# Kernel optimization log

Measured on AMD Instinct MI355X. Metric: run time of the kernel, lower is better.

## Reference

```python
import jax, jax.numpy as jnp
import numpy as np

B, P, CIN = 512, 64, 512       # batch, h*w feature positions, resnet18 channels
HID, EMB, NCLS, T = 512, 512, 96, 30


def setup_inputs() -> dict:
    key = jax.random.key(0)
    ks = jax.random.split(key, 16)
    s = 0.02
    return {
        "features": jax.random.normal(ks[0], (B, P, CIN), jnp.float32),
        "targets": jax.random.randint(ks[1], (B, T), 0, NCLS),
        "max_length": T,
        "Wfc": jax.random.normal(ks[2], (HID, CIN), jnp.float32) * s,
        "bfc": jnp.zeros((HID,), jnp.float32),
        "emb_table": jax.random.normal(ks[3], (NCLS, EMB), jnp.float32) * s,
        "Wa": jax.random.normal(ks[4], (HID, HID + EMB), jnp.float32) * s,
        "ba": jnp.zeros((HID,), jnp.float32),
        "Wc": jax.random.normal(ks[5], (HID, HID + EMB), jnp.float32) * s,
        "bc": jnp.zeros((HID,), jnp.float32),
        "Wih": jax.random.normal(ks[6], (4 * HID, HID), jnp.float32) * s,
        "Whh": jax.random.normal(ks[7], (4 * HID, HID), jnp.float32) * s,
        "bih": jnp.zeros((4 * HID,), jnp.float32),
        "bhh": jnp.zeros((4 * HID,), jnp.float32),
        "Wo": jax.random.normal(ks[8], (NCLS, HID), jnp.float32) * s,
        "bo": jnp.zeros((NCLS,), jnp.float32),
    }


def reference(features, targets, max_length, Wfc, bfc, emb_table, Wa, ba,
              Wc, bc, Wih, Whh, bih, bhh, Wo, bo):
    b = features.shape[0]
    hid = Wfc.shape[0]
    feats = features @ Wfc.T + bfc                       # [b, P, hid]
    # teacher forcing: input at t=0 is token 0, then targets[:, t-1]
    in_ids = jnp.concatenate(
        [jnp.zeros((b, 1), targets.dtype), targets[:, : max_length - 1]], axis=1)
    emb_seq = emb_table[in_ids].transpose(1, 0, 2)       # [T, b, emb]

    def step(carry, emb):
        h, c = carry
        # first softmax is over the hidden dim (as in the original module)
        a = jax.nn.softmax(jnp.concatenate([h, emb], -1) @ Wa.T + ba, axis=-1)  # [b,hid]
        scores = jnp.einsum('bph,bh->bp', feats, a)      # [b, P]
        w = jax.nn.softmax(scores, axis=-1)
        ctx = jnp.einsum('bp,bph->bh', w, feats)         # [b, hid]
        x = jnp.concatenate([emb, ctx], -1) @ Wc.T + bc  # [b, hid]
        gates = x @ Wih.T + bih + h @ Whh.T + bhh        # [b, 4*hid]
        i, f, g, o = jnp.split(gates, 4, axis=-1)        # torch gate order i,f,g,o
        c_new = jax.nn.sigmoid(f) * c + jax.nn.sigmoid(i) * jnp.tanh(g)
        h_new = jax.nn.sigmoid(o) * jnp.tanh(c_new)
        out = h_new @ Wo.T + bo                          # [b, ncls]
        return (h_new, c_new), out

    h0 = jnp.zeros((b, hid), feats.dtype)
    (_, _), outs = jax.lax.scan(step, (h0, h0), emb_seq)
    return outs.transpose(1, 0, 2)                       # [b, T, ncls]
```

## Files before the change

kernel.cpp:

```cpp
#include <hip/hip_runtime.h>
#include <math.h>

static constexpr int BATCH = 512;
static constexpr int PPOS  = 64;
static constexpr int HIDC  = 512;

typedef __attribute__((ext_vector_type(8))) short bf8;
typedef __attribute__((ext_vector_type(4))) float f4;

static __device__ __forceinline__ float sigmoidf_(float x) { return 1.f / (1.f + expf(-x)); }

static __device__ __forceinline__ short f2bf(float x) {
  unsigned u = __float_as_uint(x);
  u = u + 0x7FFF + ((u >> 16) & 1);
  return (short)(u >> 16);
}
static __device__ __forceinline__ float bf2f(short s) {
  return __uint_as_float(((unsigned)(unsigned short)s) << 16);
}

__global__ void transpose_k(const float* __restrict__ src, float* __restrict__ dst, int R, int C, int ld) {
  __shared__ float tile[32][33];
  int c0 = blockIdx.x * 32, r0 = blockIdx.y * 32;
  int x = threadIdx.x;
  for (int yy = threadIdx.y; yy < 32; yy += 8) {
    int r = r0 + yy, c = c0 + x;
    if (r < R && c < C) tile[yy][x] = src[(size_t)r * ld + c];
  }
  __syncthreads();
  for (int yy = threadIdx.y; yy < 32; yy += 8) {
    int c = c0 + yy, r = r0 + x;
    if (r < R && c < C) dst[(size_t)c * R + r] = tile[x][yy];
  }
}

__global__ void bfuse_k(const float* __restrict__ Wih, const float* __restrict__ bc,
                        const float* __restrict__ bih, const float* __restrict__ bhh,
                        float* __restrict__ bf) {
  int n = blockIdx.x * 256 + threadIdx.x;
  float s = bih[n] + bhh[n];
  const float* w = Wih + (size_t)n * 512;
  for (int m = 0; m < 512; m++) s += w[m] * bc[m];
  bf[n] = s;
}

__global__ void split_k(const float* __restrict__ src, short* __restrict__ hi, short* __restrict__ lo, int n) {
  int i = blockIdx.x * 256 + threadIdx.x;
  if (i < n) {
    float x = src[i];
    short h = f2bf(x);
    hi[i] = h;
    lo[i] = f2bf(x - bf2f(h));
  }
}

__global__ void pack_split_k(const float* __restrict__ src, int ld,
                             short* __restrict__ hi, short* __restrict__ lo) {
  int idx = blockIdx.x * 256 + threadIdx.x;
  int j = idx & 7, lane = (idx >> 3) & 63, kf = (idx >> 9) & 15, cg = idx >> 13;
  int n = cg * 16 + (lane & 15);
  int k = kf * 32 + ((lane >> 4) << 3) + j;
  float v = src[(size_t)n * ld + k];
  short h = f2bf(v);
  hi[idx] = h;
  lo[idx] = f2bf(v - bf2f(h));
}

__global__ void build_btg_pack_k(const float* __restrict__ tmp, const float* __restrict__ Whh,
                                 short* __restrict__ hi, short* __restrict__ lo) {
  int idx = blockIdx.x * 256 + threadIdx.x;
  int j = idx & 7, lane = (idx >> 3) & 63, kf = (idx >> 9) & 31, cg = idx >> 14;
  int cp = cg * 16 + (lane & 15);
  int k = kf * 32 + ((lane >> 4) << 3) + j;
  int jj = cp >> 2, g = cp & 3;
  int n = g * 512 + jj;
  float v = (k < 512) ? tmp[(size_t)(512 + k) * 2048 + n] : Whh[(size_t)n * 512 + (k - 512)];
  short h = f2bf(v);
  hi[idx] = h;
  lo[idx] = f2bf(v - bf2f(h));
}

__global__ __launch_bounds__(256) void gemb_k(const float* __restrict__ emb_table, const float* __restrict__ tmp,
                                              const float* __restrict__ bfused, float* __restrict__ Gemb_p) {
  __shared__ float emb_s[4][512];
  int tid = threadIdx.x;
  int n0 = blockIdx.x * 256;
  int e0 = blockIdx.y * 4;
  for (int i = tid; i < 2048; i += 256)
    emb_s[i >> 9][i & 511] = emb_table[(size_t)(e0 + (i >> 9)) * 512 + (i & 511)];
  __syncthreads();
  int n = n0 + tid;
  float acc[4] = {};
  for (int k = 0; k < 512; k++) {
    float w = tmp[(size_t)k * 2048 + n];
#pragma unroll
    for (int e = 0; e < 4; e++) acc[e] += emb_s[e][k] * w;
  }
  int cp = (n & 511) * 4 + (n >> 9);
  float b = bfused[n];
#pragma unroll
  for (int e = 0; e < 4; e++) Gemb_p[(size_t)(e0 + e) * 2048 + cp] = acc[e] + b;
}

__global__ __launch_bounds__(256) void za_k(const float* __restrict__ emb_table, const float* __restrict__ WaT_emb,
                                            const float* __restrict__ ba, float* __restrict__ Za) {
  __shared__ float emb_s[4][512];
  int tid = threadIdx.x;
  int n0 = blockIdx.x * 256;
  int e0 = blockIdx.y * 4;
  for (int i = tid; i < 2048; i += 256)
    emb_s[i >> 9][i & 511] = emb_table[(size_t)(e0 + (i >> 9)) * 512 + (i & 511)];
  __syncthreads();
  int n = n0 + tid;
  float acc[4] = {};
  for (int k = 0; k < 512; k++) {
    float w = WaT_emb[(size_t)k * 512 + n];
#pragma unroll
    for (int e = 0; e < 4; e++) acc[e] += emb_s[e][k] * w;
  }
  float b = ba[n];
#pragma unroll
  for (int e = 0; e < 4; e++) Za[(size_t)(e0 + e) * 512 + n] = acc[e] + b;
}

__global__ __launch_bounds__(256) void feats_mfma_k(const float* __restrict__ A,
                                                    const short* __restrict__ Ph, const short* __restrict__ Pl,
                                                    const float* __restrict__ bias, float* __restrict__ C) {
  __shared__ short Ah[2][64][40], Al[2][64][40];
  int blk = blockIdx.x;
  int xt = (blk >> 3) & 3;
  int ytile = (blk >> 5) * 8 + (blk & 7);
  int row0 = ytile * 64, col0 = xt * 128;
  int tid = threadIdx.x;
  int lane = tid & 63, wave = tid >> 6;
  int wm = (wave & 1) * 32, wn = (wave >> 1) * 64;
  int r15 = lane & 15, q8 = (lane >> 4) * 8;
  int smA = tid >> 2, skA = (tid & 3) * 8;
  const float* Ap = A + (size_t)(row0 + smA) * 512 + skA;
  int cg0 = (col0 + wn) >> 4;
  const short* pbh = Ph + (size_t)cg0 * 8192 + lane * 8;
  const short* pbl = Pl + (size_t)cg0 * 8192 + lane * 8;
  float4 a0 = *(const float4*)Ap, a1 = *(const float4*)(Ap + 4);
  bf8 bhc[4], blc[4], bhn[4], bln[4];
#pragma unroll
  for (int c = 0; c < 4; c++) {
    bhc[c] = *(const bf8*)(pbh + c * 8192);
    blc[c] = *(const bf8*)(pbl + c * 8192);
  }
  f4 acc[2][4] = {};
#pragma unroll 2
  for (int kt = 0; kt < 16; kt++) {
    int buf = kt & 1;
    {
      float av[8] = {a0.x, a0.y, a0.z, a0.w, a1.x, a1.y, a1.z, a1.w};
      bf8 ahv, alv;
#pragma unroll
      for (int i = 0; i < 8; i++) {
        short h = f2bf(av[i]);
        ahv[i] = h;
        alv[i] = f2bf(av[i] - bf2f(h));
      }
      *(bf8*)&Ah[buf][smA][skA] = ahv;
      *(bf8*)&Al[buf][smA][skA] = alv;
    }
    if (kt + 1 < 16) {
      Ap += 32;
      a0 = *(const float4*)Ap; a1 = *(const float4*)(Ap + 4);
#pragma unroll
      for (int c = 0; c < 4; c++) {
        bhn[c] = *(const bf8*)(pbh + c * 8192 + (kt + 1) * 512);
        bln[c] = *(const bf8*)(pbl + c * 8192 + (kt + 1) * 512);
      }
    }
    __syncthreads();
    bf8 fah[2], fal[2];
#pragma unroll
    for (int r = 0; r < 2; r++) {
      fah[r] = *(const bf8*)&Ah[buf][wm + r * 16 + r15][q8];
      fal[r] = *(const bf8*)&Al[buf][wm + r * 16 + r15][q8];
    }
#pragma unroll
    for (int r = 0; r < 2; r++)
#pragma unroll
      for (int c = 0; c < 4; c++) {
        acc[r][c] = __builtin_amdgcn_mfma_f32_16x16x32_bf16(fah[r], bhc[c], acc[r][c], 0, 0, 0);
        acc[r][c] = __builtin_amdgcn_mfma_f32_16x16x32_bf16(fal[r], bhc[c], acc[r][c], 0, 0, 0);
        acc[r][c] = __builtin_amdgcn_mfma_f32_16x16x32_bf16(fah[r], blc[c], acc[r][c], 0, 0, 0);
      }
#pragma unroll
    for (int c = 0; c < 4; c++) { bhc[c] = bhn[c]; blc[c] = bln[c]; }
  }
#pragma unroll
  for (int r = 0; r < 2; r++)
#pragma unroll
    for (int c = 0; c < 4; c++) {
      int col = col0 + wn + c * 16 + r15;
      float bv = bias[col];
#pragma unroll
      for (int i = 0; i < 4; i++) {
        int row = row0 + wm + r * 16 + (lane >> 4) * 4 + i;
        C[(size_t)row * 512 + col] = acc[r][c][i] + bv;
      }
    }
}

__global__ __launch_bounds__(256) void tmp_mfma_k(const float* __restrict__ A,
                                                  const short* __restrict__ BTh, const short* __restrict__ BTl,
                                                  float* __restrict__ C) {
  __shared__ short Ah[2][64][40], Al[2][64][40], Bh[2][128][40], Bl[2][128][40];
  int row0 = blockIdx.y * 64, col0 = blockIdx.x * 128;
  int tid = threadIdx.x;
  int lane = tid & 63, wave = tid >> 6;
  int wm = (wave & 1) * 32, wn = (wave >> 1) * 64;
  int r15 = lane & 15, q8 = (lane >> 4) * 8;
  int smA = tid >> 2, skA = (tid & 3) * 8;
  int smB = tid >> 1, skB = (tid & 1) * 16;
  const float* Ap = A + (size_t)(row0 + smA) * 512 + skA;
  const short* Bhp = BTh + (size_t)(col0 + smB) * 512 + skB;
  const short* Blp = BTl + (size_t)(col0 + smB) * 512 + skB;
  float4 a0 = *(const float4*)Ap, a1 = *(const float4*)(Ap + 4);
  bf8 bh0 = *(const bf8*)Bhp, bh1 = *(const bf8*)(Bhp + 8);
  bf8 bl0 = *(const bf8*)Blp, bl1 = *(const bf8*)(Blp + 8);
  f4 acc[2][4] = {};
  for (int kt = 0; kt < 16; kt++) {
    int buf = kt & 1;
    {
      float av[8] = {a0.x, a0.y, a0.z, a0.w, a1.x, a1.y, a1.z, a1.w};
      bf8 ahv, alv;
#pragma unroll
      for (int i = 0; i < 8; i++) {
        short h = f2bf(av[i]);
        ahv[i] = h;
        alv[i] = f2bf(av[i] - bf2f(h));
      }
      *(bf8*)&Ah[buf][smA][skA] = ahv;
      *(bf8*)&Al[buf][smA][skA] = alv;
      *(bf8*)&Bh[buf][smB][skB] = bh0;
      *(bf8*)&Bh[buf][smB][skB + 8] = bh1;
      *(bf8*)&Bl[buf][smB][skB] = bl0;
      *(bf8*)&Bl[buf][smB][skB + 8] = bl1;
    }
    if (kt + 1 < 16) {
      Ap += 32; Bhp += 32; Blp += 32;
      a0 = *(const float4*)Ap; a1 = *(const float4*)(Ap + 4);
      bh0 = *(const bf8*)Bhp; bh1 = *(const bf8*)(Bhp + 8);
      bl0 = *(const bf8*)Blp; bl1 = *(const bf8*)(Blp + 8);
    }
    __syncthreads();
    bf8 fah[2], fal[2], fbh[4], fbl[4];
#pragma unroll
    for (int r = 0; r < 2; r++) {
      fah[r] = *(const bf8*)&Ah[buf][wm + r * 16 + r15][q8];
      fal[r] = *(const bf8*)&Al[buf][wm + r * 16 + r15][q8];
    }
#pragma unroll
    for (int c = 0; c < 4; c++) {
      fbh[c] = *(const bf8*)&Bh[buf][wn + c * 16 + r15][q8];
      fbl[c] = *(const bf8*)&Bl[buf][wn + c * 16 + r15][q8];
    }
#pragma unroll
    for (int r = 0; r < 2; r++)
#pragma unroll
      for (int c = 0; c < 4; c++) {
        acc[r][c] = __builtin_amdgcn_mfma_f32_16x16x32_bf16(fah[r], fbh[c], acc[r][c], 0, 0, 0);
        acc[r][c] = __builtin_amdgcn_mfma_f32_16x16x32_bf16(fal[r], fbh[c], acc[r][c], 0, 0, 0);
        acc[r][c] = __builtin_amdgcn_mfma_f32_16x16x32_bf16(fah[r], fbl[c], acc[r][c], 0, 0, 0);
      }
  }
#pragma unroll
  for (int r = 0; r < 2; r++)
#pragma unroll
    for (int c = 0; c < 4; c++) {
      int col = col0 + wn + c * 16 + r15;
#pragma unroll
      for (int i = 0; i < 4; i++) {
        int row = row0 + wm + r * 16 + (lane >> 4) * 4 + i;
        C[(size_t)row * 2048 + col] = acc[r][c][i];
      }
    }
}

__global__ __launch_bounds__(256) void z_mfma_k(const short* __restrict__ h_hi, const short* __restrict__ h_lo,
                                                const short* __restrict__ Ph, const short* __restrict__ Pl,
                                                float* __restrict__ zbuf) {
  __shared__ short Ah[2][32][72], Al[2][32][72];
  int tid = threadIdx.x;
  int lane = tid & 63, wave = tid >> 6;
  int wm = (wave & 1) * 16, wn = (wave >> 1) * 16;
  int r15 = lane & 15, q4 = (lane >> 4) * 4, q8 = (lane >> 4) * 8;
  int row0 = blockIdx.y * 32, col0 = blockIdx.x * 32;
  int kz = blockIdx.z * 256;
  int sm = tid >> 3, sk = (tid & 7) * 8;
  const short* ahp = h_hi + (size_t)(row0 + sm) * 512 + kz + sk;
  const short* alp = h_lo + (size_t)(row0 + sm) * 512 + kz + sk;
  int cg = (col0 + wn) >> 4;
  const short* pbh = Ph + (size_t)cg * 8192 + (size_t)blockIdx.z * 8 * 512 + lane * 8;
  const short* pbl = Pl + (size_t)cg * 8192 + (size_t)blockIdx.z * 8 * 512 + lane * 8;
  bf8 ah = *(const bf8*)ahp, al = *(const bf8*)alp;
  bf8 bhc[2], blc[2], bhn[2], bln[2];
#pragma unroll
  for (int ks = 0; ks < 2; ks++) {
    bhc[ks] = *(const bf8*)(pbh + ks * 512);
    blc[ks] = *(const bf8*)(pbl + ks * 512);
  }
  f4 acc = {};
#pragma unroll 2
  for (int kt = 0; kt < 4; kt++) {
    int buf = kt & 1;
    *(bf8*)&Ah[buf][sm][sk] = ah;
    *(bf8*)&Al[buf][sm][sk] = al;
    if (kt + 1 < 4) {
      ahp += 64; alp += 64;
      ah = *(const bf8*)ahp; al = *(const bf8*)alp;
#pragma unroll
      for (int ks = 0; ks < 2; ks++) {
        bhn[ks] = *(const bf8*)(pbh + ((kt + 1) * 2 + ks) * 512);
        bln[ks] = *(const bf8*)(pbl + ((kt + 1) * 2 + ks) * 512);
      }
    }
    __syncthreads();
#pragma unroll
    for (int ks = 0; ks < 2; ks++) {
      bf8 fah = *(const bf8*)&Ah[buf][wm + r15][ks * 32 + q8];
      bf8 fal = *(const bf8*)&Al[buf][wm + r15][ks * 32 + q8];
      acc = __builtin_amdgcn_mfma_f32_16x16x32_bf16(fah, bhc[ks], acc, 0, 0, 0);
      acc = __builtin_amdgcn_mfma_f32_16x16x32_bf16(fal, bhc[ks], acc, 0, 0, 0);
      acc = __builtin_amdgcn_mfma_f32_16x16x32_bf16(fah, blc[ks], acc, 0, 0, 0);
    }
#pragma unroll
    for (int ks = 0; ks < 2; ks++) { bhc[ks] = bhn[ks]; blc[ks] = bln[ks]; }
  }
  float* zo = zbuf + (size_t)blockIdx.z * (512 * 512);
  int col = col0 + wn + r15;
#pragma unroll
  for (int i = 0; i < 4; i++)
    zo[(size_t)(row0 + wm + q4 + i) * 512 + col] = acc[i];
}

__global__ __launch_bounds__(512) void attn_fin_k(const float* __restrict__ zbuf,
                                                  const int* __restrict__ targets, int t, int T,
                                                  const float* __restrict__ Za, const float* __restrict__ feats,
                                                  short* __restrict__ ctx_hi, short* __restrict__ ctx_lo) {
  __shared__ float a_s[512];
  __shared__ float redm[8], reds[8];
  __shared__ float sc_s[64];
  __shared__ float w_s[64];
  __shared__ float cpart[8][512];
  int tid = threadIdx.x;
  int wid = tid >> 6, lane = tid & 63;
  int b = blockIdx.x;
  int id = (t == 0) ? 0 : targets[b * T + t - 1];

  const float4* fbase = (const float4*)(feats + (size_t)b * PPOS * 512);
  float4 f1[8], f2[8];
#pragma unroll
  for (int q = 0; q < 8; q++) {
    int p = wid * 8 + q;
    f1[q] = fbase[(size_t)p * 128 + lane];
    f2[q] = fbase[(size_t)p * 128 + 64 + lane];
  }

  float zv = zbuf[(size_t)b * 512 + tid] + zbuf[(size_t)(512 * 512) + b * 512 + tid]
           + Za[(size_t)id * 512 + tid];
  float m = zv;
#pragma unroll
  for (int off = 32; off; off >>= 1) m = fmaxf(m, __shfl_xor(m, off, 64));
  if (lane == 0) redm[wid] = m;
  __syncthreads();
  float M = redm[0];
#pragma unroll
  for (int w = 1; w < 8; w++) M = fmaxf(M, redm[w]);
  float e = expf(zv - M);
  float s = e;
#pragma unroll
  for (int off = 32; off; off >>= 1) s += __shfl_xor(s, off, 64);
  if (lane == 0) reds[wid] = s;
  __syncthreads();
  float S = 0.f;
#pragma unroll
  for (int w = 0; w < 8; w++) S += reds[w];
  a_s[tid] = e * (1.f / S);
  __syncthreads();

  float4 a1 = ((const float4*)a_s)[lane];
  float4 a2 = ((const float4*)a_s)[lane + 64];
#pragma unroll
  for (int q = 0; q < 8; q++) {
    float d = f1[q].x * a1.x + f1[q].y * a1.y + f1[q].z * a1.z + f1[q].w * a1.w
            + f2[q].x * a2.x + f2[q].y * a2.y + f2[q].z * a2.z + f2[q].w * a2.w;
#pragma unroll
    for (int off = 32; off; off >>= 1) d += __shfl_xor(d, off, 64);
    if (lane == 0) sc_s[wid * 8 + q] = d;
  }
  __syncthreads();

  if (wid == 0) {
    float v = sc_s[lane];
    float mm = v;
#pragma unroll
    for (int off = 32; off; off >>= 1) mm = fmaxf(mm, __shfl_xor(mm, off, 64));
    float ee = expf(v - mm);
    float ss = ee;
#pragma unroll
    for (int off = 32; off; off >>= 1) ss += __shfl_xor(ss, off, 64);
    w_s[lane] = ee / ss;
  }
  __syncthreads();

  float4 c1 = {0.f, 0.f, 0.f, 0.f}, c2 = {0.f, 0.f, 0.f, 0.f};
#pragma unroll
  for (int q = 0; q < 8; q++) {
    float wp = w_s[wid * 8 + q];
    c1.x += wp * f1[q].x; c1.y += wp * f1[q].y; c1.z += wp * f1[q].z; c1.w += wp * f1[q].w;
    c2.x += wp * f2[q].x; c2.y += wp * f2[q].y; c2.z += wp * f2[q].z; c2.w += wp * f2[q].w;
  }
  ((float4*)&cpart[wid][0])[lane] = c1;
  ((float4*)&cpart[wid][256])[lane] = c2;
  __syncthreads();

  float acc = 0.f;
#pragma unroll
  for (int w = 0; w < 8; w++) acc += cpart[w][tid];
  short hh = f2bf(acc);
  ctx_hi[(size_t)b * 512 + tid] = hh;
  ctx_lo[(size_t)b * 512 + tid] = f2bf(acc - bf2f(hh));
}

__global__ __launch_bounds__(256) void gates_mfma_k(const short* __restrict__ ctx_hi, const short* __restrict__ ctx_lo,
                                                    const short* __restrict__ h_hi_in, const short* __restrict__ h_lo_in,
                                                    const int* __restrict__ targets, int t, int T,
                                                    const short* __restrict__ Ph, const short* __restrict__ Pl,
                                                    const float* __restrict__ Gemb_p,
                                                    float* __restrict__ cbuf, float* __restrict__ h_new,
                                                    short* __restrict__ h_hi_out, short* __restrict__ h_lo_out) {
  __shared__ short Ah[2][32][72], Al[2][32][72];
  __shared__ float Cs[32][68];
  int tid = threadIdx.x;
  int lane = tid & 63, wave = tid >> 6;
  int wn = wave * 16;
  int r15 = lane & 15, q8 = (lane >> 4) * 8;
  int row0 = blockIdx.y * 32, col0 = blockIdx.x * 64;
  int smA = tid >> 3, skA = (tid & 7) * 8;
  const short* actx_h = ctx_hi + (size_t)(row0 + smA) * 512;
  const short* actx_l = ctx_lo + (size_t)(row0 + smA) * 512;
  const short* ahst_h = h_hi_in + (size_t)(row0 + smA) * 512;
  const short* ahst_l = h_lo_in + (size_t)(row0 + smA) * 512;
  int cg = (col0 >> 4) + wave;
  const short* pbh = Ph + (size_t)cg * 16384 + lane * 8;
  const short* pbl = Pl + (size_t)cg * 16384 + lane * 8;
  bf8 ah = *(const bf8*)(actx_h + skA), al = *(const bf8*)(actx_l + skA);
  bf8 bhc[2], blc[2], bhn[2], bln[2];
#pragma unroll
  for (int ks = 0; ks < 2; ks++) {
    bhc[ks] = *(const bf8*)(pbh + ks * 512);
    blc[ks] = *(const bf8*)(pbl + ks * 512);
  }
  f4 acc[2] = {};
#pragma unroll 2
  for (int kt = 0; kt < 16; kt++) {
    int buf = kt & 1;
    *(bf8*)&Ah[buf][smA][skA] = ah;
    *(bf8*)&Al[buf][smA][skA] = al;
    if (kt + 1 < 16) {
      int kk = (kt + 1) * 64 + skA;
      if (kk < 512) {
        ah = *(const bf8*)(actx_h + kk);
        al = *(const bf8*)(actx_l + kk);
      } else {
        ah = *(const bf8*)(ahst_h + kk - 512);
        al = *(const bf8*)(ahst_l + kk - 512);
      }
#pragma unroll
      for (int ks = 0; ks < 2; ks++) {
        bhn[ks] = *(const bf8*)(pbh + ((kt + 1) * 2 + ks) * 512);
        bln[ks] = *(const bf8*)(pbl + ((kt + 1) * 2 + ks) * 512);
      }
    }
    __syncthreads();
#pragma unroll
    for (int ks = 0; ks < 2; ks++) {
      bf8 fah[2], fal[2];
#pragma unroll
      for (int r = 0; r < 2; r++) {
        fah[r] = *(const bf8*)&Ah[buf][r * 16 + r15][ks * 32 + q8];
        fal[r] = *(const bf8*)&Al[buf][r * 16 + r15][ks * 32 + q8];
      }
#pragma unroll
      for (int r = 0; r < 2; r++) {
        acc[r] = __builtin_amdgcn_mfma_f32_16x16x32_bf16(fah[r], bhc[ks], acc[r], 0, 0, 0);
        acc[r] = __builtin_amdgcn_mfma_f32_16x16x32_bf16(fal[r], bhc[ks], acc[r], 0, 0, 0);
        acc[r] = __builtin_amdgcn_mfma_f32_16x16x32_bf16(fah[r], blc[ks], acc[r], 0, 0, 0);
      }
    }
#pragma unroll
    for (int ks = 0; ks < 2; ks++) { bhc[ks] = bhn[ks]; blc[ks] = bln[ks]; }
  }
#pragma unroll
  for (int r = 0; r < 2; r++)
#pragma unroll
    for (int i = 0; i < 4; i++)
      Cs[r * 16 + (lane >> 4) * 4 + i][wn + r15] = acc[r][i];
  __syncthreads();
#pragma unroll
  for (int it = 0; it < 2; it++) {
    int idx = it * 256 + tid;
    int row = idx >> 4, jj = idx & 15;
    int b = row0 + row;
    int jg = (col0 >> 2) + jj;
    int id = (t == 0) ? 0 : targets[b * T + t - 1];
    float4 g4 = *(const float4*)(Gemb_p + (size_t)id * 2048 + col0 + jj * 4);
    float ig = sigmoidf_(Cs[row][jj * 4 + 0] + g4.x);
    float fg = sigmoidf_(Cs[row][jj * 4 + 1] + g4.y);
    float gg = tanhf(Cs[row][jj * 4 + 2] + g4.z);
    float og = sigmoidf_(Cs[row][jj * 4 + 3] + g4.w);
    float cn = fg * cbuf[(size_t)b * 512 + jg] + ig * gg;
    float hn = og * tanhf(cn);
    cbuf[(size_t)b * 512 + jg] = cn;
    h_new[(size_t)b * 512 + jg] = hn;
    short hh = f2bf(hn);
    h_hi_out[(size_t)b * 512 + jg] = hh;
    h_lo_out[(size_t)b * 512 + jg] = f2bf(hn - bf2f(hh));
  }
}

__global__ __launch_bounds__(256) void out_gemm_k(const float* __restrict__ h_hist, const float* __restrict__ WoT,
                                                  const float* __restrict__ bo, float* __restrict__ out, int T) {
  __shared__ float As[16][68];
  __shared__ float Bs[16][96];
  int tid = threadIdx.x;
  int tx = tid & 15, ty = tid >> 4;
  int row0 = blockIdx.x * 64;
  float acc[4][6] = {};
  for (int k0 = 0; k0 < 512; k0 += 16) {
    {
      int r = tid >> 2;
      int kk = (tid & 3) * 4;
      float4 v = *(const float4*)(h_hist + (size_t)(row0 + r) * 512 + k0 + kk);
      As[kk + 0][r] = v.x; As[kk + 1][r] = v.y; As[kk + 2][r] = v.z; As[kk + 3][r] = v.w;
    }
#pragma unroll
    for (int i = 0; i < 6; i++) {
      int e = tid + 256 * i;
      int kb = e / 96, n = e - kb * 96;
      Bs[kb][n] = WoT[(size_t)(k0 + kb) * 96 + n];
    }
    __syncthreads();
#pragma unroll
    for (int q = 0; q < 16; q++) {
      float av[4], bvv[6];
#pragma unroll
      for (int i = 0; i < 4; i++) av[i] = As[q][ty * 4 + i];
#pragma unroll
      for (int j = 0; j < 6; j++) bvv[j] = Bs[q][tx * 6 + j];
#pragma unroll
      for (int i = 0; i < 4; i++)
#pragma unroll
        for (int j = 0; j < 6; j++) acc[i][j] += av[i] * bvv[j];
    }
    __syncthreads();
  }
#pragma unroll
  for (int i = 0; i < 4; i++)
#pragma unroll
    for (int j = 0; j < 6; j++) {
      int row = row0 + ty * 4 + i;
      int tt = row >> 9, bb = row & 511;
      int cc = tx * 6 + j;
      out[((size_t)bb * T + tt) * 96 + cc] = acc[i][j] + bo[cc];
    }
}

extern "C" void kernel_launch(void* const* d_in, const int* in_sizes, int n_in,
                              void* d_out, int out_size, void* d_ws, size_t ws_size,
                              hipStream_t stream) {
  const float* features  = (const float*)d_in[0];
  const int*   targets   = (const int*)d_in[1];
  const float* Wfc       = (const float*)d_in[3];
  const float* bfc       = (const float*)d_in[4];
  const float* emb_table = (const float*)d_in[5];
  const float* Wa        = (const float*)d_in[6];
  const float* ba        = (const float*)d_in[7];
  const float* Wc        = (const float*)d_in[8];
  const float* bc        = (const float*)d_in[9];
  const float* Wih       = (const float*)d_in[10];
  const float* Whh       = (const float*)d_in[11];
  const float* bih       = (const float*)d_in[12];
  const float* bhh       = (const float*)d_in[13];
  const float* Wo        = (const float*)d_in[14];
  const float* bo        = (const float*)d_in[15];
  float* out = (float*)d_out;
  int T = in_sizes[1] / BATCH;

  char* base = (char*)d_ws;
  auto alloc = [&](size_t bytes) -> char* {
    char* p = base;
    base += (bytes + 255) & ~(size_t)255;
    return p;
  };
  float* feats   = (float*)alloc((size_t)BATCH * PPOS * HIDC * 4);
  float* WaT_emb = (float*)alloc(512 * 512 * 4);
  float* WcT     = (float*)alloc(1024 * 512 * 4);
  float* tmp     = (float*)alloc((size_t)1024 * 2048 * 4);
  short* Wih_hi  = (short*)alloc((size_t)2048 * 512 * 2);
  short* Wih_lo  = (short*)alloc((size_t)2048 * 512 * 2);
  short* PBTg_hi = (short*)alloc((size_t)2048 * 1024 * 2);
  short* PBTg_lo = (short*)alloc((size_t)2048 * 1024 * 2);
  short* Pfc_hi  = (short*)alloc(512 * 512 * 2);
  short* Pfc_lo  = (short*)alloc(512 * 512 * 2);
  short* Pwa_hi  = (short*)alloc(512 * 512 * 2);
  short* Pwa_lo  = (short*)alloc(512 * 512 * 2);
  float* Gemb_p  = (float*)alloc(96 * 2048 * 4);
  float* Za      = (float*)alloc(96 * 512 * 4);
  float* bfused  = (float*)alloc(2048 * 4);
  float* WoT     = (float*)alloc(512 * 96 * 4);
  float* cbuf    = (float*)alloc(BATCH * HIDC * 4);
  float* zbuf    = (float*)alloc((size_t)2 * BATCH * HIDC * 4);
  short* ctx_hi  = (short*)alloc(BATCH * HIDC * 2);
  short* ctx_lo  = (short*)alloc(BATCH * HIDC * 2);
  short* h_hi    = (short*)alloc(BATCH * HIDC * 2);
  short* h_lo    = (short*)alloc(BATCH * HIDC * 2);
  float* h_hist  = (float*)alloc((size_t)T * BATCH * HIDC * 4);

  dim3 tb(32, 8);
  transpose_k<<<dim3(16, 16), tb, 0, stream>>>(Wa + 512, WaT_emb, 512, 512, 1024);
  transpose_k<<<dim3(32, 16), tb, 0, stream>>>(Wc, WcT, 512, 1024, 1024);
  transpose_k<<<dim3(16, 3),  tb, 0, stream>>>(Wo, WoT, 96, 512, 512);

  split_k<<<(2048 * 512) / 256, 256, 0, stream>>>(Wih, Wih_hi, Wih_lo, 2048 * 512);
  pack_split_k<<<(512 * 512) / 256, 256, 0, stream>>>(Wfc, 512, Pfc_hi, Pfc_lo);
  pack_split_k<<<(512 * 512) / 256, 256, 0, stream>>>(Wa, 1024, Pwa_hi, Pwa_lo);

  tmp_mfma_k<<<dim3(16, 16), 256, 0, stream>>>(WcT, Wih_hi, Wih_lo, tmp);

  bfuse_k<<<8, 256, 0, stream>>>(Wih, bc, bih, bhh, bfused);
  build_btg_pack_k<<<(2048 * 1024) / 256, 256, 0, stream>>>(tmp, Whh, PBTg_hi, PBTg_lo);
  gemb_k<<<dim3(8, 24), 256, 0, stream>>>(emb_table, tmp, bfused, Gemb_p);
  za_k<<<dim3(2, 24), 256, 0, stream>>>(emb_table, WaT_emb, ba, Za);

  feats_mfma_k<<<2048, 256, 0, stream>>>(features, Pfc_hi, Pfc_lo, bfc, feats);

  hipMemsetAsync(cbuf, 0, (size_t)BATCH * HIDC * 4, stream);
  hipMemsetAsync(h_hi, 0, (size_t)BATCH * HIDC * 2, stream);
  hipMemsetAsync(h_lo, 0, (size_t)BATCH * HIDC * 2, stream);

  for (int t = 0; t < T; t++) {
    float* h_new = h_hist + (size_t)t * BATCH * HIDC;
    z_mfma_k<<<dim3(16, 16, 2), 256, 0, stream>>>(h_hi, h_lo, Pwa_hi, Pwa_lo, zbuf);
    attn_fin_k<<<512, 512, 0, stream>>>(zbuf, targets, t, T, Za, feats, ctx_hi, ctx_lo);
    gates_mfma_k<<<dim3(32, 16), 256, 0, stream>>>(ctx_hi, ctx_lo, h_hi, h_lo, targets, t, T,
                                                   PBTg_hi, PBTg_lo, Gemb_p, cbuf, h_new, h_hi, h_lo);
  }
  out_gemm_k<<<(T * BATCH) / 64, 256, 0, stream>>>(h_hist, WoT, bo, out, T);
}
```

Measured before the change: 1.335 ms.

## Load MFMA A-fragments directly from global memory, dropping LDS staging

A new kernel pre-splits the features tensor into bf16 hi/lo arrays. The feats GEMM and the per-step z GEMM now load A fragments straight from global memory into registers, with a register prefetch, and no longer stage them through LDS with __syncthreads. This removes LDS traffic and block barriers, and z_mfma_k runs in all 30 timesteps. The cost is an extra full pass that writes 64MB of split features, and A fragments that were shared through LDS are now loaded redundantly by several waves from global or cache.

```diff
diff --git a/kernel.cpp b/kernel.cpp
--- a/kernel.cpp
+++ b/kernel.cpp
@@ -6,6 +6,7 @@
 static constexpr int HIDC  = 512;
 
 typedef __attribute__((ext_vector_type(8))) short bf8;
+typedef __attribute__((ext_vector_type(4))) short s4v;
 typedef __attribute__((ext_vector_type(4))) float f4;
 
 static __device__ __forceinline__ float sigmoidf_(float x) { return 1.f / (1.f + expf(-x)); }
@@ -52,6 +53,21 @@
     hi[i] = h;
     lo[i] = f2bf(x - bf2f(h));
   }
+}
+
+__global__ void fsplit_k(const float* __restrict__ src, short* __restrict__ hi, short* __restrict__ lo) {
+  int i = blockIdx.x * 256 + threadIdx.x;
+  float4 v = ((const float4*)src)[i];
+  float a[4] = {v.x, v.y, v.z, v.w};
+  s4v h4, l4;
+#pragma unroll
+  for (int j = 0; j < 4; j++) {
+    short h = f2bf(a[j]);
+    h4[j] = h;
+    l4[j] = f2bf(a[j] - bf2f(h));
+  }
+  ((s4v*)hi)[i] = h4;
+  ((s4v*)lo)[i] = l4;
 }
 
 __global__ void pack_split_k(const float* __restrict__ src, int ld,
@@ -123,10 +139,9 @@
   for (int e = 0; e < 4; e++) Za[(size_t)(e0 + e) * 512 + n] = acc[e] + b;
 }
 
-__global__ __launch_bounds__(256) void feats_mfma_k(const float* __restrict__ A,
+__global__ __launch_bounds__(256) void feats_mfma_k(const short* __restrict__ Fh, const short* __restrict__ Fl,
                                                     const short* __restrict__ Ph, const short* __restrict__ Pl,
                                                     const float* __restrict__ bias, float* __restrict__ C) {
-  __shared__ short Ah[2][64][40], Al[2][64][40];
   int blk = blockIdx.x;
   int xt = (blk >> 3) & 3;
   int ytile = (blk >> 5) * 8 + (blk & 7);
@@ -135,60 +150,44 @@
   int lane = tid & 63, wave = tid >> 6;
   int wm = (wave & 1) * 32, wn = (wave >> 1) * 64;
   int r15 = lane & 15, q8 = (lane >> 4) * 8;
-  int smA = tid >> 2, skA = (tid & 3) * 8;
-  const float* Ap = A + (size_t)(row0 + smA) * 512 + skA;
+  const short* a0h = Fh + (size_t)(row0 + wm + r15) * 512 + q8;
+  const short* a0l = Fl + (size_t)(row0 + wm + r15) * 512 + q8;
   int cg0 = (col0 + wn) >> 4;
   const short* pbh = Ph + (size_t)cg0 * 8192 + lane * 8;
   const short* pbl = Pl + (size_t)cg0 * 8192 + lane * 8;
-  float4 a0 = *(const float4*)Ap, a1 = *(const float4*)(Ap + 4);
-  bf8 bhc[4], blc[4], bhn[4], bln[4];
+  bf8 cah[2], cal[2], cbh[4], cbl[4], nah[2], nal[2], nbh[4], nbl[4];
+  cah[0] = *(const bf8*)a0h; cah[1] = *(const bf8*)(a0h + 16 * 512);
+  cal[0] = *(const bf8*)a0l; cal[1] = *(const bf8*)(a0l + 16 * 512);
 #pragma unroll
   for (int c = 0; c < 4; c++) {
-    bhc[c] = *(const bf8*)(pbh + c * 8192);
-    blc[c] = *(const bf8*)(pbl + c * 8192);
+    cbh[c] = *(const bf8*)(pbh + c * 8192);
+    cbl[c] = *(const bf8*)(pbl + c * 8192);
   }
   f4 acc[2][4] = {};
-#pragma unroll 2
+#pragma unroll 4
   for (int kt = 0; kt < 16; kt++) {
-    int buf = kt & 1;
-    {
-      float av[8] = {a0.x, a0.y, a0.z, a0.w, a1.x, a1.y, a1.z, a1.w};
-      bf8 ahv, alv;
-#pragma unroll
-      for (int i = 0; i < 8; i++) {
-        short h = f2bf(av[i]);
-        ahv[i] = h;
-        alv[i] = f2bf(av[i] - bf2f(h));
-      }
-      *(bf8*)&Ah[buf][smA][skA] = ahv;
-      *(bf8*)&Al[buf][smA][skA] = alv;
-    }
     if (kt + 1 < 16) {
-      Ap += 32;
-      a0 = *(const float4*)Ap; a1 = *(const float4*)(Ap + 4);
+      int o = (kt + 1) * 32;
+      nah[0] = *(const bf8*)(a0h + o); nah[1] = *(const bf8*)(a0h + 16 * 512 + o);
+      nal[0] = *(const bf8*)(a0l + o); nal[1] = *(const bf8*)(a0l + 16 * 512 + o);
 #pragma unroll
       for (int c = 0; c < 4; c++) {
-        bhn[c] = *(const bf8*)(pbh + c * 8192 + (kt + 1) * 512);
-        bln[c] = *(const bf8*)(pbl + c * 8192 + (kt + 1) * 512);
-      }
-    }
-    __syncthreads();
-    bf8 fah[2], fal[2];
-#pragma unroll
-    for (int r = 0; r < 2; r++) {
-      fah[r] = *(const bf8*)&Ah[buf][wm + r * 16 + r15][q8];
-      fal[r] = *(const bf8*)&Al[buf][wm + r * 16 + r15][q8];
+        nbh[c] = *(const bf8*)(pbh + c * 8192 + (kt + 1) * 512);
+        nbl[c] = *(const bf8*)(pbl + c * 8192 + (kt + 1) * 512);
+      }
     }
 #pragma unroll
     for (int r = 0; r < 2; r++)
 #pragma unroll
       for (int c = 0; c < 4; c++) {
-        acc[r][c] = __builtin_amdgcn_mfma_f32_16x16x32_bf16(fah[r], bhc[c], acc[r][c], 0, 0, 0);
-        acc[r][c] = __builtin_amdgcn_mfma_f32_16x16x32_bf16(fal[r], bhc[c], acc[r][c], 0, 0, 0);
-        acc[r][c] = __builtin_amdgcn_mfma_f32_16x16x32_bf16(fah[r], blc[c], acc[r][c], 0, 0, 0);
-      }
-#pragma unroll
-    for (int c = 0; c < 4; c++) { bhc[c] = bhn[c]; blc[c] = bln[c]; }
+        acc[r][c] = __builtin_amdgcn_mfma_f32_16x16x32_bf16(cah[r], cbh[c], acc[r][c], 0, 0, 0);
+        acc[r][c] = __builtin_amdgcn_mfma_f32_16x16x32_bf16(cal[r], cbh[c], acc[r][c], 0, 0, 0);
+        acc[r][c] = __builtin_amdgcn_mfma_f32_16x16x32_bf16(cah[r], cbl[c], acc[r][c], 0, 0, 0);
+      }
+#pragma unroll
+    for (int r = 0; r < 2; r++) { cah[r] = nah[r]; cal[r] = nal[r]; }
+#pragma unroll
+    for (int c = 0; c < 4; c++) { cbh[c] = nbh[c]; cbl[c] = nbl[c]; }
   }
 #pragma unroll
   for (int r = 0; r < 2; r++)
@@ -283,52 +282,33 @@
 __global__ __launch_bounds__(256) void z_mfma_k(const short* __restrict__ h_hi, const short* __restrict__ h_lo,
                                                 const short* __restrict__ Ph, const short* __restrict__ Pl,
                                                 float* __restrict__ zbuf) {
-  __shared__ short Ah[2][32][72], Al[2][32][72];
   int tid = threadIdx.x;
   int lane = tid & 63, wave = tid >> 6;
   int wm = (wave & 1) * 16, wn = (wave >> 1) * 16;
   int r15 = lane & 15, q4 = (lane >> 4) * 4, q8 = (lane >> 4) * 8;
   int row0 = blockIdx.y * 32, col0 = blockIdx.x * 32;
   int kz = blockIdx.z * 256;
-  int sm = tid >> 3, sk = (tid & 7) * 8;
-  const short* ahp = h_hi + (size_t)(row0 + sm) * 512 + kz + sk;
-  const short* alp = h_lo + (size_t)(row0 + sm) * 512 + kz + sk;
+  const short* ah = h_hi + (size_t)(row0 + wm + r15) * 512 + kz + q8;
+  const short* al = h_lo + (size_t)(row0 + wm + r15) * 512 + kz + q8;
   int cg = (col0 + wn) >> 4;
-  const short* pbh = Ph + (size_t)cg * 8192 + (size_t)blockIdx.z * 8 * 512 + lane * 8;
-  const short* pbl = Pl + (size_t)cg * 8192 + (size_t)blockIdx.z * 8 * 512 + lane * 8;
-  bf8 ah = *(const bf8*)ahp, al = *(const bf8*)alp;
-  bf8 bhc[2], blc[2], bhn[2], bln[2];
-#pragma unroll
-  for (int ks = 0; ks < 2; ks++) {
-    bhc[ks] = *(const bf8*)(pbh + ks * 512);
-    blc[ks] = *(const bf8*)(pbl + ks * 512);
-  }
+  const short* pbh = Ph + (size_t)cg * 8192 + (size_t)blockIdx.z * 4096 + lane * 8;
+  const short* pbl = Pl + (size_t)cg * 8192 + (size_t)blockIdx.z * 4096 + lane * 8;
+  bf8 cah = *(const bf8*)ah, cal = *(const bf8*)al;
+  bf8 cbh = *(const bf8*)pbh, cbl = *(const bf8*)pbl;
+  bf8 nah, nal, nbh, nbl;
   f4 acc = {};
-#pragma unroll 2
-  for (int kt = 0; kt < 4; kt++) {
-    int buf = kt & 1;
-    *(bf8*)&Ah[buf][sm][sk] = ah;
-    *(bf8*)&Al[buf][sm][sk] = al;
-    if (kt + 1 < 4) {
-      ahp += 64; alp += 64;
-      ah = *(const bf8*)ahp; al = *(const bf8*)alp;
-#pragma unroll
-      for (int ks = 0; ks < 2; ks++) {
-        bhn[ks] = *(const bf8*)(pbh + ((kt + 1) * 2 + ks) * 512);
-        bln[ks] = *(const bf8*)(pbl + ((kt + 1) * 2 + ks) * 512);
-      }
-    }
-    __syncthreads();
-#pragma unroll
-    for (int ks = 0; ks < 2; ks++) {
-      bf8 fah = *(const bf8*)&Ah[buf][wm + r15][ks * 32 + q8];
-      bf8 fal = *(const bf8*)&Al[buf][wm + r15][ks * 32 + q8];
-      acc = __builtin_amdgcn_mfma_f32_16x16x32_bf16(fah, bhc[ks], acc, 0, 0, 0);
-      acc = __builtin_amdgcn_mfma_f32_16x16x32_bf16(fal, bhc[ks], acc, 0, 0, 0);
-      acc = __builtin_amdgcn_mfma_f32_16x16x32_bf16(fah, blc[ks], acc, 0, 0, 0);
-    }
-#pragma unroll
-    for (int ks = 0; ks < 2; ks++) { bhc[ks] = bhn[ks]; blc[ks] = bln[ks]; }
+#pragma unroll
+  for (int kt = 0; kt < 8; kt++) {
+    if (kt + 1 < 8) {
+      nah = *(const bf8*)(ah + (kt + 1) * 32);
+      nal = *(const bf8*)(al + (kt + 1) * 32);
+      nbh = *(const bf8*)(pbh + (kt + 1) * 512);
+      nbl = *(const bf8*)(pbl + (kt + 1) * 512);
+    }
+    acc = __builtin_amdgcn_mfma_f32_16x16x32_bf16(cah, cbh, acc, 0, 0, 0);
+    acc = __builtin_amdgcn_mfma_f32_16x16x32_bf16(cal, cbh, acc, 0, 0, 0);
+    acc = __builtin_amdgcn_mfma_f32_16x16x32_bf16(cah, cbl, acc, 0, 0, 0);
+    cah = nah; cal = nal; cbh = nbh; cbl = nbl;
   }
   float* zo = zbuf + (size_t)blockIdx.z * (512 * 512);
   int col = col0 + wn + r15;
@@ -598,6 +578,8 @@
     return p;
   };
   float* feats   = (float*)alloc((size_t)BATCH * PPOS * HIDC * 4);
+  short* f_hi    = (short*)alloc((size_t)BATCH * PPOS * HIDC * 2);
+  short* f_lo    = (short*)alloc((size_t)BATCH * PPOS * HIDC * 2);
   float* WaT_emb = (float*)alloc(512 * 512 * 4);
   float* WcT     = (float*)alloc(1024 * 512 * 4);
   float* tmp     = (float*)alloc((size_t)1024 * 2048 * 4);
@@ -629,6 +611,7 @@
   split_k<<<(2048 * 512) / 256, 256, 0, stream>>>(Wih, Wih_hi, Wih_lo, 2048 * 512);
   pack_split_k<<<(512 * 512) / 256, 256, 0, stream>>>(Wfc, 512, Pfc_hi, Pfc_lo);
   pack_split_k<<<(512 * 512) / 256, 256, 0, stream>>>(Wa, 1024, Pwa_hi, Pwa_lo);
+  fsplit_k<<<(BATCH * PPOS * HIDC / 4) / 256, 256, 0, stream>>>(features, f_hi, f_lo);
 
   tmp_mfma_k<<<dim3(16, 16), 256, 0, stream>>>(WcT, Wih_hi, Wih_lo, tmp);
 
@@ -637,7 +620,7 @@
   gemb_k<<<dim3(8, 24), 256, 0, stream>>>(emb_table, tmp, bfused, Gemb_p);
   za_k<<<dim3(2, 24), 256, 0, stream>>>(emb_table, WaT_emb, ba, Za);
 
-  feats_mfma_k<<<2048, 256, 0, stream>>>(features, Pfc_hi, Pfc_lo, bfc, feats);
+  feats_mfma_k<<<2048, 256, 0, stream>>>(f_hi, f_lo, Pfc_hi, Pfc_lo, bfc, feats);
 
   hipMemsetAsync(cbuf, 0, (size_t)BATCH * HIDC * 4, stream);
   hipMemsetAsync(h_hi, 0, (size_t)BATCH * HIDC * 2, stream);
```

Measured after the change: 1.448 ms. 8.5% more time.
